# Optimization experiments

Measured on AMD Instinct MI355X. Metric: run time of the kernel, lower is better.

Reference implementation:

```python
import jax, jax.numpy as jnp
import numpy as np

B = 262144
SLOPE = 0.2

def _xavier(key, shape):
    # shape = (out_ch, in_ch, k); fan_in = in_ch*k, fan_out = out_ch*k
    fan_in = shape[1] * shape[2]
    fan_out = shape[0] * shape[2]
    limit = np.sqrt(6.0 / (fan_in + fan_out)).astype(np.float32)
    return jax.random.uniform(key, shape, jnp.float32, -limit, limit)

def setup_inputs() -> dict:
    key = jax.random.key(0)
    ks = jax.random.split(key, 5)
    x = jax.random.normal(ks[0], (B, 2, 16), jnp.float32)
    return {
        "x": x,
        "w_enc1": _xavier(ks[1], (4, 2, 3)), "b_enc1": jnp.zeros((4,), jnp.float32),
        "w_bneck": _xavier(ks[2], (8, 4, 3)), "b_bneck": jnp.zeros((8,), jnp.float32),
        "w_dec1": _xavier(ks[3], (4, 8, 3)), "b_dec1": jnp.zeros((4,), jnp.float32),
        "w_out": _xavier(ks[4], (2, 4, 3)), "b_out": jnp.zeros((2,), jnp.float32),
    }

def _conv1d(x, w, b, stride):
    # x: [B, C_in, L], w: [C_out, C_in, K], padding=1
    y = jax.lax.conv_general_dilated(
        x, w, window_strides=(stride,), padding=[(1, 1)],
        dimension_numbers=("NCH", "OIH", "NCH"))
    return y + b[None, :, None]

def _leaky(y):
    return jnp.where(y > 0, y, SLOPE * y)

def _upsample2(y):
    # nearest-neighbor x2 along length
    return jnp.repeat(y, 2, axis=-1)

def reference(x, w_enc1, b_enc1, w_bneck, b_bneck, w_dec1, b_dec1, w_out, b_out):
    enc1 = _leaky(_conv1d(x, w_enc1, b_enc1, 2))          # [B,4,8]
    bneck = _leaky(_conv1d(enc1, w_bneck, b_bneck, 2))    # [B,8,4]
    up1 = _upsample2(bneck)                               # [B,8,8]
    dec1 = _leaky(_conv1d(up1, w_dec1, b_dec1, 1))        # [B,4,8]
    skip = dec1 + enc1                                    # [B,4,8]
    up2 = _upsample2(skip)                                # [B,4,16]
    out = jnp.tanh(_conv1d(up2, w_out, b_out, 1))         # [B,2,16]
    return out
```

## Files before the change

kernel.cpp:

```cpp
#include <hip/hip_runtime.h>

typedef float v2f __attribute__((ext_vector_type(2)));

#define SLOPE 0.2f

static __device__ __forceinline__ v2f leaky2(v2f v) {
    return __builtin_elementwise_max(v, SLOPE * v);
}

static __device__ __forceinline__ v2f fma2(v2f a, v2f b, v2f c) {
    return __builtin_elementwise_fma(a, b, c);
}

static __device__ __forceinline__ float fast_tanh(float v) {
    float e = __expf(2.0f * v);
    return 1.0f - 2.0f * __builtin_amdgcn_rcpf(e + 1.0f);
}

__global__ __launch_bounds__(64, 4) void minigen_kernel(
    const float* __restrict__ x,
    const float* __restrict__ w1, const float* __restrict__ b1,
    const float* __restrict__ w2, const float* __restrict__ b2,
    const float* __restrict__ w3, const float* __restrict__ b3,
    const float* __restrict__ w4, const float* __restrict__ b4,
    float* __restrict__ out)
{
    __shared__ float4 lds[64 * 9];

    const int t = threadIdx.x;
    const int blockBase = blockIdx.x * 512;

    const float4* xin = (const float4*)x;
#pragma unroll
    for (int q = 0; q < 8; ++q) {
        int g = q * 64 + t;
        lds[(g >> 3) * 9 + (g & 7)] = xin[blockBase + g];
    }

    float xr[2][16];
#pragma unroll
    for (int m = 0; m < 8; ++m) {
        float4 v = lds[t * 9 + m];
        int c = m >> 2, base = (m & 3) * 4;
        xr[c][base+0] = v.x; xr[c][base+1] = v.y;
        xr[c][base+2] = v.z; xr[c][base+3] = v.w;
    }

    v2f e1p[2][8];
#pragma unroll
    for (int cp = 0; cp < 2; ++cp) {
#pragma unroll
        for (int l = 0; l < 8; ++l) {
            v2f s = { b1[2*cp], b1[2*cp+1] };
#pragma unroll
            for (int ic = 0; ic < 2; ++ic)
#pragma unroll
                for (int k = 0; k < 3; ++k) {
                    int u = 2*l - 1 + k;
                    if (u >= 0) {
                        v2f w = { w1[((2*cp)*2 + ic)*3 + k],
                                  w1[((2*cp+1)*2 + ic)*3 + k] };
                        float xv = xr[ic][u];
                        s = fma2(w, (v2f){xv, xv}, s);
                    }
                }
            e1p[cp][l] = leaky2(s);
        }
    }

    v2f bnp[4][4];
#pragma unroll
    for (int cp = 0; cp < 4; ++cp) {
#pragma unroll
        for (int l = 0; l < 4; ++l) {
            v2f s = { b2[2*cp], b2[2*cp+1] };
#pragma unroll
            for (int ic = 0; ic < 4; ++ic)
#pragma unroll
                for (int k = 0; k < 3; ++k) {
                    int u = 2*l - 1 + k;
                    if (u >= 0) {
                        float ev = (ic & 1) ? e1p[ic>>1][u].y
                                            : e1p[ic>>1][u].x;
                        v2f w = { w2[((2*cp)*4 + ic)*3 + k],
                                  w2[((2*cp+1)*4 + ic)*3 + k] };
                        s = fma2(w, (v2f){ev, ev}, s);
                    }
                }
            bnp[cp][l] = leaky2(s);
        }
    }

    v2f skp[2][8];
#pragma unroll
    for (int cp = 0; cp < 2; ++cp) {
#pragma unroll
        for (int l = 0; l < 8; ++l) {
            v2f s = { b3[2*cp], b3[2*cp+1] };
#pragma unroll
            for (int ic = 0; ic < 8; ++ic)
#pragma unroll
                for (int k = 0; k < 3; ++k) {
                    int u = l - 1 + k;
                    if (u >= 0 && u < 8) {
                        int j = u >> 1;
                        float bv = (ic & 1) ? bnp[ic>>1][j].y
                                            : bnp[ic>>1][j].x;
                        v2f w = { w3[((2*cp)*8 + ic)*3 + k],
                                  w3[((2*cp+1)*8 + ic)*3 + k] };
                        s = fma2(w, (v2f){bv, bv}, s);
                    }
                }
            skp[cp][l] = leaky2(s) + e1p[cp][l];
        }
    }

    v2f op4[16];
#pragma unroll
    for (int l = 0; l < 16; ++l) {
        v2f s = { b4[0], b4[1] };
#pragma unroll
        for (int ic = 0; ic < 4; ++ic)
#pragma unroll
            for (int k = 0; k < 3; ++k) {
                int u = l - 1 + k;
                if (u >= 0 && u < 16) {
                    int j = u >> 1;
                    float sv = (ic & 1) ? skp[ic>>1][j].y
                                        : skp[ic>>1][j].x;
                    v2f w = { w4[(0*4 + ic)*3 + k],
                              w4[(1*4 + ic)*3 + k] };
                    s = fma2(w, (v2f){sv, sv}, s);
                }
            }
        op4[l] = (v2f){ fast_tanh(s.x), fast_tanh(s.y) };
    }

#pragma unroll
    for (int m = 0; m < 4; ++m) {
        lds[t*9 + m]     = make_float4(op4[4*m+0].x, op4[4*m+1].x,
                                       op4[4*m+2].x, op4[4*m+3].x);
        lds[t*9 + 4 + m] = make_float4(op4[4*m+0].y, op4[4*m+1].y,
                                       op4[4*m+2].y, op4[4*m+3].y);
    }

    float4* outp = (float4*)out;
#pragma unroll
    for (int q = 0; q < 8; ++q) {
        int g = q * 64 + t;
        outp[blockBase + g] = lds[(g >> 3) * 9 + (g & 7)];
    }
}

extern "C" void kernel_launch(void* const* d_in, const int* in_sizes, int n_in,
                              void* d_out, int out_size, void* d_ws, size_t ws_size,
                              hipStream_t stream) {
    const float* x  = (const float*)d_in[0];
    const float* w1 = (const float*)d_in[1];
    const float* b1 = (const float*)d_in[2];
    const float* w2 = (const float*)d_in[3];
    const float* b2 = (const float*)d_in[4];
    const float* w3 = (const float*)d_in[5];
    const float* b3 = (const float*)d_in[6];
    const float* w4 = (const float*)d_in[7];
    const float* b4 = (const float*)d_in[8];
    float* out = (float*)d_out;

    int n = in_sizes[0] / 32;
    int grid = n / 64;
    hipLaunchKernelGGL(minigen_kernel, dim3(grid), dim3(64), 0, stream,
                       x, w1, b1, w2, b2, w3, b3, w4, b4, out);
}
```

Baseline: 106.8 us.

## Split each sample across two lanes with shuffle-based halo exchange

Each sample is now processed by two adjacent lanes, each computing half of the sequence length, with boundary values exchanged through xor-1 wave shuffles at each conv stage. Blocks now cover 32 samples instead of 64, which doubles the grid and halves LDS per block, and the launch-bounds occupancy hint rises from 4 to 6. The aim is lower per-thread register pressure and more waves in flight to hide memory latency. The cost is extra shuffle and select instructions plus some redundant halo arithmetic.

```diff
diff --git a/kernel.cpp b/kernel.cpp
--- a/kernel.cpp
+++ b/kernel.cpp
@@ -17,7 +17,14 @@
     return 1.0f - 2.0f * __builtin_amdgcn_rcpf(e + 1.0f);
 }
 
-__global__ __launch_bounds__(64, 4) void minigen_kernel(
+static __device__ __forceinline__ v2f shfl_xor1(v2f v) {
+    v2f r;
+    r.x = __shfl_xor(v.x, 1, 64);
+    r.y = __shfl_xor(v.y, 1, 64);
+    return r;
+}
+
+__global__ __launch_bounds__(64, 6) void minigen_kernel(
     const float* __restrict__ x,
     const float* __restrict__ w1, const float* __restrict__ b1,
     const float* __restrict__ w2, const float* __restrict__ b2,
@@ -25,128 +32,157 @@
     const float* __restrict__ w4, const float* __restrict__ b4,
     float* __restrict__ out)
 {
-    __shared__ float4 lds[64 * 9];
+    __shared__ float4 lds[32 * 9];
 
     const int t = threadIdx.x;
-    const int blockBase = blockIdx.x * 512;
+    const int s = t >> 1;
+    const int h = t & 1;
+    const int blockBase = blockIdx.x * 256;
 
     const float4* xin = (const float4*)x;
 #pragma unroll
-    for (int q = 0; q < 8; ++q) {
+    for (int q = 0; q < 4; ++q) {
         int g = q * 64 + t;
         lds[(g >> 3) * 9 + (g & 7)] = xin[blockBase + g];
     }
 
-    float xr[2][16];
-#pragma unroll
-    for (int m = 0; m < 8; ++m) {
-        float4 v = lds[t * 9 + m];
-        int c = m >> 2, base = (m & 3) * 4;
-        xr[c][base+0] = v.x; xr[c][base+1] = v.y;
-        xr[c][base+2] = v.z; xr[c][base+3] = v.w;
-    }
-
-    v2f e1p[2][8];
-#pragma unroll
-    for (int cp = 0; cp < 2; ++cp) {
-#pragma unroll
-        for (int l = 0; l < 8; ++l) {
-            v2f s = { b1[2*cp], b1[2*cp+1] };
+    const float* slab = (const float*)lds;
+    float xw[2][9];
+#pragma unroll
+    for (int c = 0; c < 2; ++c) {
+        float4 a = lds[s*9 + c*4 + 2*h];
+        float4 b = lds[s*9 + c*4 + 2*h + 1];
+        float gr = slab[s*36 + c*16 + 7];
+        xw[c][0] = h ? gr : 0.0f;
+        xw[c][1]=a.x; xw[c][2]=a.y; xw[c][3]=a.z; xw[c][4]=a.w;
+        xw[c][5]=b.x; xw[c][6]=b.y; xw[c][7]=b.z; xw[c][8]=b.w;
+    }
+
+    v2f e1p[2][4];
+#pragma unroll
+    for (int cp = 0; cp < 2; ++cp) {
+#pragma unroll
+        for (int ll = 0; ll < 4; ++ll) {
+            v2f acc = { b1[2*cp], b1[2*cp+1] };
 #pragma unroll
             for (int ic = 0; ic < 2; ++ic)
 #pragma unroll
                 for (int k = 0; k < 3; ++k) {
-                    int u = 2*l - 1 + k;
-                    if (u >= 0) {
-                        v2f w = { w1[((2*cp)*2 + ic)*3 + k],
-                                  w1[((2*cp+1)*2 + ic)*3 + k] };
-                        float xv = xr[ic][u];
-                        s = fma2(w, (v2f){xv, xv}, s);
-                    }
+                    int lu = 2*ll + k;
+                    v2f w = { w1[((2*cp)*2 + ic)*3 + k],
+                              w1[((2*cp+1)*2 + ic)*3 + k] };
+                    float xv = xw[ic][lu];
+                    acc = fma2(w, (v2f){xv, xv}, acc);
                 }
-            e1p[cp][l] = leaky2(s);
+            e1p[cp][ll] = leaky2(acc);
         }
     }
 
-    v2f bnp[4][4];
+    v2f e1g[2];
+#pragma unroll
+    for (int cp = 0; cp < 2; ++cp) {
+        v2f r = shfl_xor1(e1p[cp][3]);
+        e1g[cp] = h ? r : (v2f){0.0f, 0.0f};
+    }
+
+    v2f bnp[4][2];
 #pragma unroll
     for (int cp = 0; cp < 4; ++cp) {
 #pragma unroll
-        for (int l = 0; l < 4; ++l) {
-            v2f s = { b2[2*cp], b2[2*cp+1] };
+        for (int ll = 0; ll < 2; ++ll) {
+            v2f acc = { b2[2*cp], b2[2*cp+1] };
 #pragma unroll
             for (int ic = 0; ic < 4; ++ic)
 #pragma unroll
                 for (int k = 0; k < 3; ++k) {
-                    int u = 2*l - 1 + k;
-                    if (u >= 0) {
-                        float ev = (ic & 1) ? e1p[ic>>1][u].y
-                                            : e1p[ic>>1][u].x;
-                        v2f w = { w2[((2*cp)*4 + ic)*3 + k],
-                                  w2[((2*cp+1)*4 + ic)*3 + k] };
-                        s = fma2(w, (v2f){ev, ev}, s);
-                    }
+                    int lw = 2*ll + k;
+                    int icp = ic >> 1;
+                    v2f col = (lw == 0) ? e1g[icp] : e1p[icp][lw-1];
+                    float ev = (ic & 1) ? col.y : col.x;
+                    v2f w = { w2[((2*cp)*4 + ic)*3 + k],
+                              w2[((2*cp+1)*4 + ic)*3 + k] };
+                    acc = fma2(w, (v2f){ev, ev}, acc);
                 }
-            bnp[cp][l] = leaky2(s);
+            bnp[cp][ll] = leaky2(acc);
         }
     }
 
-    v2f skp[2][8];
-#pragma unroll
-    for (int cp = 0; cp < 2; ++cp) {
-#pragma unroll
-        for (int l = 0; l < 8; ++l) {
-            v2f s = { b3[2*cp], b3[2*cp+1] };
+    v2f bg0[4], bg3[4];
+#pragma unroll
+    for (int cp = 0; cp < 4; ++cp) {
+        v2f r1 = shfl_xor1(bnp[cp][1]);
+        v2f r0 = shfl_xor1(bnp[cp][0]);
+        bg0[cp] = h ? r1 : (v2f){0.0f, 0.0f};
+        bg3[cp] = h ? (v2f){0.0f, 0.0f} : r0;
+    }
+
+    v2f skp[2][4];
+#pragma unroll
+    for (int cp = 0; cp < 2; ++cp) {
+#pragma unroll
+        for (int ll = 0; ll < 4; ++ll) {
+            v2f acc = { b3[2*cp], b3[2*cp+1] };
 #pragma unroll
             for (int ic = 0; ic < 8; ++ic)
 #pragma unroll
                 for (int k = 0; k < 3; ++k) {
-                    int u = l - 1 + k;
-                    if (u >= 0 && u < 8) {
-                        int j = u >> 1;
-                        float bv = (ic & 1) ? bnp[ic>>1][j].y
-                                            : bnp[ic>>1][j].x;
-                        v2f w = { w3[((2*cp)*8 + ic)*3 + k],
-                                  w3[((2*cp+1)*8 + ic)*3 + k] };
-                        s = fma2(w, (v2f){bv, bv}, s);
-                    }
+                    int c3 = ll - 1 + k;
+                    int jw = (c3 < 0) ? 0 : (c3 >> 1) + 1;
+                    int icp = ic >> 1;
+                    v2f col = (jw == 0) ? bg0[icp]
+                            : (jw == 3) ? bg3[icp]
+                            : bnp[icp][jw-1];
+                    float bv = (ic & 1) ? col.y : col.x;
+                    v2f w = { w3[((2*cp)*8 + ic)*3 + k],
+                              w3[((2*cp+1)*8 + ic)*3 + k] };
+                    acc = fma2(w, (v2f){bv, bv}, acc);
                 }
-            skp[cp][l] = leaky2(s) + e1p[cp][l];
+            skp[cp][ll] = leaky2(acc) + e1p[cp][ll];
         }
     }
 
-    v2f op4[16];
-#pragma unroll
-    for (int l = 0; l < 16; ++l) {
-        v2f s = { b4[0], b4[1] };
+    v2f sg0[2], sg5[2];
+#pragma unroll
+    for (int cp = 0; cp < 2; ++cp) {
+        v2f r3 = shfl_xor1(skp[cp][3]);
+        v2f r0 = shfl_xor1(skp[cp][0]);
+        sg0[cp] = h ? r3 : (v2f){0.0f, 0.0f};
+        sg5[cp] = h ? (v2f){0.0f, 0.0f} : r0;
+    }
+
+    v2f op4[8];
+#pragma unroll
+    for (int ll = 0; ll < 8; ++ll) {
+        v2f acc = { b4[0], b4[1] };
 #pragma unroll
         for (int ic = 0; ic < 4; ++ic)
 #pragma unroll
             for (int k = 0; k < 3; ++k) {
-                int u = l - 1 + k;
-                if (u >= 0 && u < 16) {
-                    int j = u >> 1;
-                    float sv = (ic & 1) ? skp[ic>>1][j].y
-                                        : skp[ic>>1][j].x;
-                    v2f w = { w4[(0*4 + ic)*3 + k],
-                              w4[(1*4 + ic)*3 + k] };
-                    s = fma2(w, (v2f){sv, sv}, s);
-                }
+                int c4 = ll - 1 + k;
+                int jw = (c4 < 0) ? 0 : (c4 >> 1) + 1;
+                int icp = ic >> 1;
+                v2f col = (jw == 0) ? sg0[icp]
+                        : (jw == 5) ? sg5[icp]
+                        : skp[icp][jw-1];
+                float sv = (ic & 1) ? col.y : col.x;
+                v2f w = { w4[(0*4 + ic)*3 + k],
+                          w4[(1*4 + ic)*3 + k] };
+                acc = fma2(w, (v2f){sv, sv}, acc);
             }
-        op4[l] = (v2f){ fast_tanh(s.x), fast_tanh(s.y) };
-    }
-
-#pragma unroll
-    for (int m = 0; m < 4; ++m) {
-        lds[t*9 + m]     = make_float4(op4[4*m+0].x, op4[4*m+1].x,
-                                       op4[4*m+2].x, op4[4*m+3].x);
-        lds[t*9 + 4 + m] = make_float4(op4[4*m+0].y, op4[4*m+1].y,
-                                       op4[4*m+2].y, op4[4*m+3].y);
+        op4[ll] = (v2f){ fast_tanh(acc.x), fast_tanh(acc.y) };
+    }
+
+#pragma unroll
+    for (int m = 0; m < 2; ++m) {
+        lds[s*9 + 2*h + m]     = make_float4(op4[4*m+0].x, op4[4*m+1].x,
+                                             op4[4*m+2].x, op4[4*m+3].x);
+        lds[s*9 + 4 + 2*h + m] = make_float4(op4[4*m+0].y, op4[4*m+1].y,
+                                             op4[4*m+2].y, op4[4*m+3].y);
     }
 
     float4* outp = (float4*)out;
 #pragma unroll
-    for (int q = 0; q < 8; ++q) {
+    for (int q = 0; q < 4; ++q) {
         int g = q * 64 + t;
         outp[blockBase + g] = lds[(g >> 3) * 9 + (g & 7)];
     }
@@ -166,8 +202,8 @@
     const float* b4 = (const float*)d_in[8];
     float* out = (float*)d_out;
 
-    int n = in_sizes[0] / 32;
-    int grid = n / 64;
+    int samples = in_sizes[0] / 32;
+    int grid = samples / 32;
     hipLaunchKernelGGL(minigen_kernel, dim3(grid), dim3(64), 0, stream,
                        x, w1, b1, w2, b2, w3, b3, w4, b4, out);
 }
```

Result: slower. 111.8 us (+4.6%).
